# Optimization experiments

Measured on AMD Instinct MI355X. Metric: run time of the kernel, lower is better.

## Reference

```python
import jax, jax.numpy as jnp
import numpy as np

N_HEAD = 4
GROUPS = 32
EPS = 1e-5


def group_norm(x, scale, bias):
    B, C, H, W = x.shape
    xg = x.reshape(B, GROUPS, C // GROUPS, H, W)
    mu = xg.mean(axis=(2, 3, 4), keepdims=True)
    var = xg.var(axis=(2, 3, 4), keepdims=True)
    xg = (xg - mu) * jax.lax.rsqrt(var + EPS)
    x = xg.reshape(B, C, H, W)
    return x * scale[None, :, None, None] + bias[None, :, None, None]


def setup_inputs() -> dict:
    key = jax.random.key(0)
    k0, k1, k2 = jax.random.split(key, 3)
    B, C, H, W = 2, 64, 64, 64
    x = jax.random.normal(k0, (B, C, H, W), dtype=jnp.float32)
    gn_scale = jnp.ones((C,), dtype=jnp.float32)
    gn_bias = jnp.zeros((C,), dtype=jnp.float32)
    w_qkv = jax.random.normal(k1, (3 * C, C), dtype=jnp.float32) * 0.05  # 1x1 conv, no bias
    w_out = jax.random.normal(k2, (C, C), dtype=jnp.float32) * 0.05     # 1x1 conv
    b_out = jnp.zeros((C,), dtype=jnp.float32)
    return {"x": x, "gn_scale": gn_scale, "gn_bias": gn_bias,
            "w_qkv": w_qkv, "w_out": w_out, "b_out": b_out}


def reference(x, gn_scale, gn_bias, w_qkv, w_out, b_out):
    B, C, H, W = x.shape
    head_dim = C // N_HEAD
    norm = group_norm(x, gn_scale, gn_bias)
    # 1x1 conv == channel matmul
    qkv = jnp.einsum('oc,bchw->bohw', w_qkv, norm)
    qkv = qkv.reshape(B, N_HEAD, head_dim * 3, H, W)
    q, k, v = jnp.split(qkv, 3, axis=2)  # each [B, n, head_dim, H, W]
    # full spatial attention scores, scaled by sqrt(channel) as in source
    attn = jnp.einsum('bnchw,bncyx->bnhwyx', q, k) / jnp.sqrt(jnp.float32(C))
    attn = jax.nn.softmax(attn.reshape(B, N_HEAD, H, W, H * W), axis=-1)
    attn = attn.reshape(B, N_HEAD, H, W, H, W)
    out = jnp.einsum('bnhwyx,bncyx->bnchw', attn, v).reshape(B, C, H, W)
    out = jnp.einsum('oc,bchw->bohw', w_out, out) + b_out[None, :, None, None]
    return out + x
```

## Files before the change

kernel.cpp:

```cpp
#include <hip/hip_runtime.h>
#include <hip/hip_bf16.h>

typedef __attribute__((ext_vector_type(8))) short short8;
typedef __attribute__((ext_vector_type(4))) float f32x4;
typedef __attribute__((ext_vector_type(16))) float f32x16;
typedef __attribute__((ext_vector_type(4))) unsigned int uint4v;
typedef __attribute__((ext_vector_type(4))) unsigned short ushort4v;

#define DEV static __device__ __forceinline__

DEV unsigned short f2bf(float f){
  unsigned u = __float_as_uint(f);
  u += 0x7fffu + ((u >> 16) & 1u);
  return (unsigned short)(u >> 16);
}

DEV float bf2f(unsigned short h){
  unsigned u = ((unsigned)h) << 16;
  float f;
  __builtin_memcpy(&f, &u, 4);
  return f;
}

DEV unsigned pack2bf(float a, float b){
  __hip_bfloat162 h = __float22bfloat162_rn(make_float2(a, b));
  unsigned u;
  __builtin_memcpy(&u, &h, 4);
  return u;
}

#define QSCALE 0.180336880111f
#define NSPLIT 8
#define NT 8
#define KSTRIDE 24

__global__ __launch_bounds__(256) void gn_partial_k(const float* __restrict__ x,
                                                    float* __restrict__ gp){
  int blk = blockIdx.x;
  float4 v = ((const float4*)(x + (size_t)blk*1024))[threadIdx.x];
  float s = v.x+v.y+v.z+v.w;
  float q = v.x*v.x+v.y*v.y+v.z*v.z+v.w*v.w;
  #pragma unroll
  for (int off = 1; off < 64; off <<= 1){
    s += __shfl_xor(s, off);
    q += __shfl_xor(q, off);
  }
  __shared__ float red[8];
  int w = threadIdx.x >> 6;
  if ((threadIdx.x & 63) == 0){ red[w*2] = s; red[w*2+1] = q; }
  __syncthreads();
  if (threadIdx.x == 0){
    gp[blk*2+0] = red[0]+red[2]+red[4]+red[6];
    gp[blk*2+1] = red[1]+red[3]+red[5]+red[7];
  }
}

__global__ __launch_bounds__(256) void qkv_k(const float* __restrict__ x,
    const float* __restrict__ gp, const float* __restrict__ gsc,
    const float* __restrict__ gbi, const float* __restrict__ wq,
    unsigned short* __restrict__ q, unsigned short* __restrict__ k,
    unsigned short* __restrict__ vt){
  int b  = blockIdx.x >> 8;
  int s0 = (blockIdx.x & 255) * 16;
  __shared__ float W[192][68];
  __shared__ float A[16][68];
  __shared__ float MS[32][2];
  int t = threadIdx.x;
  for (int i = t; i < 3072; i += 256){
    int o = i >> 4, c4 = (i & 15) * 4;
    *(float4*)&W[o][c4] = ((const float4*)wq)[i];
  }
  if (t < 32){
    float s = 0.f, ss = 0.f;
    #pragma unroll
    for (int i = 0; i < 8; ++i){
      const float* pp = gp + ((b*32 + t)*8 + i)*2;
      s += pp[0]; ss += pp[1];
    }
    float mean = s * (1.f/8192.f);
    MS[t][0] = mean;
    MS[t][1] = rsqrtf(ss * (1.f/8192.f) - mean*mean + 1e-5f);
  }
  if (t < 64){
    int n = t >> 4, si = t & 15;
    vt[((size_t)(b*4 + n)*32 + 16)*4096 + s0 + si] = (unsigned short)0x3F80;
  }
  __syncthreads();
  {
    int c  = t >> 2;
    int s4 = (t & 3) * 4;
    const float* px = x + ((size_t)b*64 + c)*4096 + s0 + s4;
    float4 v0 = *(const float4*)px;
    float sc = gsc[c] * MS[c>>1][1];
    float bi = gbi[c] - MS[c>>1][0] * sc;
    A[s4+0][c]=v0.x*sc+bi; A[s4+1][c]=v0.y*sc+bi;
    A[s4+2][c]=v0.z*sc+bi; A[s4+3][c]=v0.w*sc+bi;
  }
  __syncthreads();
  int sl = t >> 4, grp = t & 15;
  float acc[12];
  #pragma unroll
  for (int j = 0; j < 12; ++j) acc[j] = 0.f;
  for (int c4 = 0; c4 < 16; ++c4){
    float4 a = *(const float4*)&A[sl][c4*4];
    #pragma unroll
    for (int j = 0; j < 12; ++j){
      float4 wv = *(const float4*)&W[grp + j*16][c4*4];
      acc[j] = fmaf(a.x, wv.x, fmaf(a.y, wv.y, fmaf(a.z, wv.z, fmaf(a.w, wv.w, acc[j]))));
    }
  }
  int s = s0 + sl;
  int slp = (sl & 0x3) | (((sl >> 2) & 1) << 3) | (((sl >> 3) & 1) << 2);
  #pragma unroll
  for (int j = 0; j < 12; ++j){
    int o = grp + j*16;
    int n = o / 48, r = o % 48;
    float val = acc[j];
    if (r < 16){
      q[(((size_t)b*4 + n)*4096 + s)*16 + r] = f2bf(val * QSCALE);
    } else if (r < 32){
      k[(((size_t)b*4 + n)*4096 + s)*16 + r - 16] = f2bf(val);
    } else {
      vt[((size_t)(b*4 + n)*32 + (r - 32))*4096 + s0 + slp] = f2bf(val);
    }
  }
}

__global__ __launch_bounds__(256, 4) void attn_k(const unsigned short* __restrict__ qb,
    const unsigned short* __restrict__ kb, const unsigned short* __restrict__ vt,
    unsigned short* __restrict__ part, float* __restrict__ lsums){
  int blk = blockIdx.x;
  int bn = blk & 7;
  int sp = (blk >> 3) & (NSPLIT - 1);
  int qg = blk >> 6;
  int t = threadIdx.x, w = t >> 6, l = t & 63;
  int lq = l & 31, hi = l >> 5;

  __shared__ unsigned short Klds[512 * KSTRIDE];

  {
    const unsigned short* ksrc = kb + ((size_t)bn*4096 + sp*512)*16;
    #pragma unroll
    for (int p = 0; p < 4; ++p){
      int g = p*256 + t;
      int r = g >> 1, h = g & 1;
      *(short8*)&Klds[r*KSTRIDE + h*8] = *(const short8*)(ksrc + (size_t)g*8);
    }
  }

  int qrow = qg*128 + w*32;
  short8 qf = *(const short8*)(qb + ((size_t)bn*4096 + qrow)*16 + (size_t)lq*16 + hi*8);

  int vrow = (lq < 16) ? lq : 16;
  const unsigned short* vaddr = vt + ((size_t)bn*32 + vrow)*4096 + sp*512 + hi*8;

  f32x16 O0, O1, zero;
  #pragma unroll
  for (int r = 0; r < 16; ++r){ O0[r] = 0.f; O1[r] = 0.f; zero[r] = 0.f; }

  __syncthreads();

  auto packP = [&](const f32x16& pc, int h8) -> short8 {
    uint4v pw;
    pw[0] = pack2bf(pc[h8+0], pc[h8+1]);
    pw[1] = pack2bf(pc[h8+2], pc[h8+3]);
    pw[2] = pack2bf(pc[h8+4], pc[h8+5]);
    pw[3] = pack2bf(pc[h8+6], pc[h8+7]);
    return __builtin_bit_cast(short8, pw);
  };

  #pragma unroll
  for (int kt = 0; kt < NT; ++kt){
    const unsigned short* va = vaddr + kt*64;
    short8 v0 = *(const short8*)(va);
    short8 v1 = *(const short8*)(va + 16);
    short8 v2 = *(const short8*)(va + 32);
    short8 v3 = *(const short8*)(va + 48);
    short8 kf0 = *(const short8*)&Klds[(kt*64 + lq)*KSTRIDE + hi*8];
    short8 kf1 = *(const short8*)&Klds[(kt*64 + 32 + lq)*KSTRIDE + hi*8];

    __builtin_amdgcn_s_setprio(1);
    f32x16 sA = __builtin_amdgcn_mfma_f32_32x32x16_bf16(kf0, qf, zero, 0, 0, 0);
    f32x16 sB = __builtin_amdgcn_mfma_f32_32x32x16_bf16(kf1, qf, zero, 0, 0, 0);
    __builtin_amdgcn_s_setprio(0);

    #pragma unroll
    for (int r = 0; r < 16; ++r) sA[r] = __builtin_amdgcn_exp2f(sA[r]);
    #pragma unroll
    for (int r = 0; r < 16; ++r) sB[r] = __builtin_amdgcn_exp2f(sB[r]);

    short8 paA0 = packP(sA, 0), paA1 = packP(sA, 8);
    short8 paB0 = packP(sB, 0), paB1 = packP(sB, 8);

    __builtin_amdgcn_s_setprio(1);
    O0 = __builtin_amdgcn_mfma_f32_32x32x16_bf16(paA0, v0, O0, 0, 0, 0);
    O1 = __builtin_amdgcn_mfma_f32_32x32x16_bf16(paA1, v1, O1, 0, 0, 0);
    O0 = __builtin_amdgcn_mfma_f32_32x32x16_bf16(paB0, v2, O0, 0, 0, 0);
    O1 = __builtin_amdgcn_mfma_f32_32x32x16_bf16(paB1, v3, O1, 0, 0, 0);
    __builtin_amdgcn_s_setprio(0);
  }

  #pragma unroll
  for (int r = 0; r < 16; ++r) O0[r] += O1[r];

  unsigned short* Op = part + (((size_t)sp*8 + bn)*4096 + qrow)*16;
  size_t lbase = ((size_t)sp*8 + bn)*4096 + qrow;
  #pragma unroll
  for (int r = 0; r < 16; ++r){
    int qr = (r&3) + 8*(r>>2) + 4*hi;
    if (lq < 16) __builtin_nontemporal_store(f2bf(O0[r]), &Op[(size_t)qr*16 + lq]);
  }
  if (lq == 16){
    #pragma unroll
    for (int r = 0; r < 16; ++r){
      int qr = (r&3) + 8*(r>>2) + 4*hi;
      __builtin_nontemporal_store(O0[r], &lsums[lbase + qr]);
    }
  }
}

__global__ __launch_bounds__(256) void oproj_k(const unsigned short* __restrict__ part,
    const float* __restrict__ lsums, const float* __restrict__ wo,
    const float* __restrict__ bo, const float* __restrict__ x,
    float* __restrict__ out){
  int b  = blockIdx.x >> 8;
  int s0 = (blockIdx.x & 255) * 16;
  __shared__ float W[64][68];
  __shared__ float A[16][68];
  int t = threadIdx.x;
  for (int i = t; i < 1024; i += 256){
    int o = i >> 4, c4 = (i & 15) * 4;
    *(float4*)&W[o][c4] = ((const float4*)wo)[i];
  }
  {
    int sl = t & 15;
    int u  = t >> 4;
    int n = u >> 2, d4 = (u & 3) * 4;
    size_t row = ((size_t)b*4 + n)*4096 + s0 + sl;
    float L = 0.f;
    #pragma unroll
    for (int sp = 0; sp < NSPLIT; ++sp)
      L += __builtin_nontemporal_load(&lsums[(size_t)sp*32768 + row]);
    f32x4 acc = {0.f,0.f,0.f,0.f};
    #pragma unroll
    for (int sp = 0; sp < NSPLIT; ++sp){
      ushort4v u0 = *(const ushort4v*)(part + ((size_t)sp*32768 + row)*16 + d4);
      acc[0] += bf2f(u0[0]); acc[1] += bf2f(u0[1]);
      acc[2] += bf2f(u0[2]); acc[3] += bf2f(u0[3]);
    }
    float inv = 1.f / L;
    A[sl][n*16+d4+0] = acc[0]*inv; A[sl][n*16+d4+1] = acc[1]*inv;
    A[sl][n*16+d4+2] = acc[2]*inv; A[sl][n*16+d4+3] = acc[3]*inv;
  }
  __syncthreads();
  int sl = t & 15, grp = t >> 4;
  float acc[4] = {0.f,0.f,0.f,0.f};
  for (int c4 = 0; c4 < 16; ++c4){
    float4 a = *(const float4*)&A[sl][c4*4];
    #pragma unroll
    for (int j = 0; j < 4; ++j){
      float4 wv = *(const float4*)&W[grp + j*16][c4*4];
      acc[j] = fmaf(a.x, wv.x, fmaf(a.y, wv.y, fmaf(a.z, wv.z, fmaf(a.w, wv.w, acc[j]))));
    }
  }
  int s = s0 + sl;
  #pragma unroll
  for (int j = 0; j < 4; ++j){
    int o = grp + j*16;
    size_t idx = ((size_t)b*64 + o)*4096 + s;
    out[idx] = acc[j] + bo[o] + x[idx];
  }
}

extern "C" void kernel_launch(void* const* d_in, const int* in_sizes, int n_in,
                              void* d_out, int out_size, void* d_ws, size_t ws_size,
                              hipStream_t stream){
  const float* x   = (const float*)d_in[0];
  const float* gsc = (const float*)d_in[1];
  const float* gbi = (const float*)d_in[2];
  const float* wq  = (const float*)d_in[3];
  const float* wo  = (const float*)d_in[4];
  const float* bo  = (const float*)d_in[5];
  float* out = (float*)d_out;

  char* ws = (char*)d_ws;
  float* gp           = (float*)ws;
  unsigned short* q   = (unsigned short*)(ws + 8192);
  unsigned short* k   = (unsigned short*)(ws + 8192 + 1048576);
  unsigned short* vt  = (unsigned short*)(ws + 8192 + 2097152);
  unsigned short* part= (unsigned short*)(ws + 8192 + 4194304);
  float* lsums        = (float*)(ws + 8192 + 4194304 + 8388608);

  gn_partial_k<<<512,  256, 0, stream>>>(x, gp);
  qkv_k       <<<512,  256, 0, stream>>>(x, gp, gsc, gbi, wq, q, k, vt);
  attn_k      <<<2048, 256, 0, stream>>>(q, k, vt, part, lsums);
  oproj_k     <<<512,  256, 0, stream>>>(part, lsums, wo, bo, x, out);
}
```

Before: 54.93 us.

## Retile QKV projection per head with 64-position tiles

The QKV projection kernel now assigns each block one (batch, head) pair and 64 spatial positions, instead of 16 positions across all 192 output channels. Each block loads only its head's 48 weight rows, which shrinks the per-block weight staging and lets it be reused over more positions. Threads map to positions, so q and k stores coalesce differently. The cost is that normalized input is recomputed once per head (4x redundant reads of x), and the launch grid must match the new indexing, which the launch site not shown here presumably handles.

Result: slower. 90.42 us, median of 2 (+64.6%).

```diff
diff --git a/kernel.cpp b/kernel.cpp
--- a/kernel.cpp
+++ b/kernel.cpp
@@ -60,15 +60,16 @@
     const float* __restrict__ gbi, const float* __restrict__ wq,
     unsigned short* __restrict__ q, unsigned short* __restrict__ k,
     unsigned short* __restrict__ vt){
-  int b  = blockIdx.x >> 8;
-  int s0 = (blockIdx.x & 255) * 16;
-  __shared__ float W[192][68];
-  __shared__ float A[16][68];
+  int bn = blockIdx.x & 7;
+  int b  = bn >> 2, n = bn & 3;
+  int s0 = (blockIdx.x >> 3) * 64;
+  __shared__ float W[48][68];
+  __shared__ float A[64][68];
   __shared__ float MS[32][2];
   int t = threadIdx.x;
-  for (int i = t; i < 3072; i += 256){
-    int o = i >> 4, c4 = (i & 15) * 4;
-    *(float4*)&W[o][c4] = ((const float4*)wq)[i];
+  for (int i = t; i < 768; i += 256){
+    int o = i >> 4, c4 = i & 15;
+    *(float4*)&W[o][c4*4] = ((const float4*)wq)[(size_t)(n*48 + o)*16 + c4];
   }
   if (t < 32){
     float s = 0.f, ss = 0.f;
@@ -81,23 +82,21 @@
     MS[t][0] = mean;
     MS[t][1] = rsqrtf(ss * (1.f/8192.f) - mean*mean + 1e-5f);
   }
-  if (t < 64){
-    int n = t >> 4, si = t & 15;
-    vt[((size_t)(b*4 + n)*32 + 16)*4096 + s0 + si] = (unsigned short)0x3F80;
-  }
-  __syncthreads();
-  {
-    int c  = t >> 2;
-    int s4 = (t & 3) * 4;
-    const float* px = x + ((size_t)b*64 + c)*4096 + s0 + s4;
-    float4 v0 = *(const float4*)px;
+  if (t < 64)
+    vt[((size_t)bn*32 + 16)*4096 + s0 + t] = (unsigned short)0x3F80;
+  __syncthreads();
+  #pragma unroll
+  for (int p = 0; p < 4; ++p){
+    int idx = p*256 + t;
+    int c = idx >> 4, g = idx & 15;
+    float4 v0 = *(const float4*)(x + ((size_t)b*64 + c)*4096 + s0 + g*4);
     float sc = gsc[c] * MS[c>>1][1];
     float bi = gbi[c] - MS[c>>1][0] * sc;
-    A[s4+0][c]=v0.x*sc+bi; A[s4+1][c]=v0.y*sc+bi;
-    A[s4+2][c]=v0.z*sc+bi; A[s4+3][c]=v0.w*sc+bi;
-  }
-  __syncthreads();
-  int sl = t >> 4, grp = t & 15;
+    A[g*4+0][c]=v0.x*sc+bi; A[g*4+1][c]=v0.y*sc+bi;
+    A[g*4+2][c]=v0.z*sc+bi; A[g*4+3][c]=v0.w*sc+bi;
+  }
+  __syncthreads();
+  int sl = t & 63, grp = t >> 6;
   float acc[12];
   #pragma unroll
   for (int j = 0; j < 12; ++j) acc[j] = 0.f;
@@ -105,23 +104,22 @@
     float4 a = *(const float4*)&A[sl][c4*4];
     #pragma unroll
     for (int j = 0; j < 12; ++j){
-      float4 wv = *(const float4*)&W[grp + j*16][c4*4];
+      float4 wv = *(const float4*)&W[grp + j*4][c4*4];
       acc[j] = fmaf(a.x, wv.x, fmaf(a.y, wv.y, fmaf(a.z, wv.z, fmaf(a.w, wv.w, acc[j]))));
     }
   }
   int s = s0 + sl;
-  int slp = (sl & 0x3) | (((sl >> 2) & 1) << 3) | (((sl >> 3) & 1) << 2);
+  int slp = (sl & 0x33) | (((sl >> 2) & 1) << 3) | (((sl >> 3) & 1) << 2);
   #pragma unroll
   for (int j = 0; j < 12; ++j){
-    int o = grp + j*16;
-    int n = o / 48, r = o % 48;
+    int r = grp + j*4;
     float val = acc[j];
     if (r < 16){
-      q[(((size_t)b*4 + n)*4096 + s)*16 + r] = f2bf(val * QSCALE);
+      q[(((size_t)bn)*4096 + s)*16 + r] = f2bf(val * QSCALE);
     } else if (r < 32){
-      k[(((size_t)b*4 + n)*4096 + s)*16 + r - 16] = f2bf(val);
+      k[(((size_t)bn)*4096 + s)*16 + r - 16] = f2bf(val);
     } else {
-      vt[((size_t)(b*4 + n)*32 + (r - 32))*4096 + s0 + slp] = f2bf(val);
+      vt[((size_t)bn*32 + (r - 32))*4096 + s0 + slp] = f2bf(val);
     }
   }
 }
```
